# Kernel tuning notes

Hardware: AMD Instinct MI355X
Metric: run time of the kernel (lower is better)

Reference implementation:

```python
import jax, jax.numpy as jnp
import numpy as np

PATCH_SIZE = 24
ALPHA = 0.2  # LeakyReLU negative slope


def setup_inputs() -> dict:
    key = jax.random.key(0)
    k_x, k_adj, k_w, k_wc = jax.random.split(key, 4)
    B, T, N, Cin, Cout = 2, 96, 64, 16, 32
    x = jax.random.normal(k_x, (B, T, N, Cin), dtype=jnp.float32)
    adj = jax.random.uniform(k_adj, (N, N), dtype=jnp.float32)  # weighted adjacency in [0,1)
    # xavier_uniform with gain=1.414 on (Cin, Cout)
    limit = 1.414 * float(np.sqrt(6.0 / (Cin + Cout)))
    W = jax.random.uniform(k_w, (Cin, Cout), dtype=jnp.float32, minval=-limit, maxval=limit)
    W_c = jax.random.uniform(k_wc, (Cout,), dtype=jnp.float32, minval=-0.1, maxval=0.1)
    return {"x": x, "adj": adj, "W": W, "W_c": W_c}


def reference(x, adj, W, W_c):
    B, T, N, Cin = x.shape
    P = PATCH_SIZE
    NP = T // P
    Cout = W.shape[1]
    # torch.view semantics == row-major jnp.reshape (faithful, even though it mixes axes)
    x_patched = x.reshape(B, NP, N, P, Cin)
    h = x_patched @ W  # (B, NP, N, P, Cout)
    # vectorized over patches: per-patch outer product over nodes
    e = jnp.einsum('bsipc,bsjpc->bsijpc', h, h)  # (B, NP, N, N, P, Cout)
    e = jnp.where(e >= 0, e, ALPHA * e)  # LeakyReLU
    e = e * adj[None, None, :, :, None, None]
    e = jax.nn.softmax(e, axis=-1)  # softmax over channel dim (as in original)
    # torch.stack(list, dim=4) of (b,i,j,p,c) over patch index -> (B,N,N,P,NP,C)
    e = jnp.transpose(e, (0, 2, 3, 4, 1, 5))
    attention = e.reshape(B, N, N, T, Cout)  # (B, N, N, T, Cout)
    # h_patched.permute(0,2,1,3,4).reshape(B,N,T,C)
    h_flat = jnp.transpose(h, (0, 2, 1, 3, 4)).reshape(B, N, T, Cout)
    # einsum('bnqtc,bntc->bntc') == sum over q then elementwise multiply
    h_prime = attention.sum(axis=2) * h_flat
    return attention, jax.nn.elu(h_prime)
```

## Files before the change

### kernel.cpp

```cpp
#include <hip/hip_runtime.h>
#include <math.h>

#define Bq 2
#define Tq 96
#define Nq 64
#define CIN 16
#define COUT 32
#define PATCH 24
#define NPq 4
#define ATT_SIZE (Bq * Nq * Nq * Tq * COUT)
#define H_ROWS (Bq * NPq * Nq * PATCH)

typedef float f4 __attribute__((ext_vector_type(4)));

__global__ __launch_bounds__(256) void h_gemm_kernel(
    const float* __restrict__ x, const float* __restrict__ W,
    float* __restrict__ h) {
    __shared__ float Wl[CIN * COUT];
    __shared__ float xs[8 * CIN];
    int tid = threadIdx.x;
    Wl[tid]       = W[tid];
    Wl[tid + 256] = W[tid + 256];
    if (tid < 8 * CIN) xs[tid] = x[blockIdx.x * (8 * CIN) + tid];
    __syncthreads();
    int rl = tid >> 5;
    int c  = tid & 31;
    float acc = 0.f;
#pragma unroll
    for (int k = 0; k < CIN; ++k)
        acc += xs[rl * CIN + k] * Wl[k * COUT + c];
    h[blockIdx.x * 256 + tid] = acc;
}

__global__ __launch_bounds__(768) void att_fused_kernel(
    const float* __restrict__ h, const float* __restrict__ adj,
    float* __restrict__ att, float* __restrict__ hprime) {
    const int bi = blockIdx.x;
    const int s  = bi & 3;
    const int i  = (bi >> 2) & 63;
    const int b  = bi >> 8;
    const int tid  = threadIdx.x;
    const int c0   = (tid & 7) * 4;
    const int p    = (tid >> 3) % PATCH;
    const int jsub = tid / 192;
    const int j0   = jsub * 16;

    __shared__ float adjrow[Nq];
    __shared__ f4 red[768];
    if (tid < Nq) adjrow[tid] = adj[i * Nq + tid];
    __syncthreads();

    const float* hb = h + (size_t)((b * NPq + s) * Nq) * (PATCH * COUT);
    const f4 hi = *(const f4*)(hb + (i * PATCH + p) * COUT + c0);

    f4 acc = {0.f, 0.f, 0.f, 0.f};
    const int t = p * NPq + s;
    size_t outbase = ((size_t)((b * Nq + i) * Nq + j0) * Tq + t) * COUT + c0;
    const size_t jstride = (size_t)Tq * COUT;

#pragma unroll 4
    for (int jj = 0; jj < 16; ++jj) {
        const f4 hj = *(const f4*)(hb + ((j0 + jj) * PATCH + p) * COUT + c0);
        const float aj = adjrow[j0 + jj];

        f4 e = hi * hj;
        e.x = fmaxf(e.x, 0.2f * e.x) * aj;
        e.y = fmaxf(e.y, 0.2f * e.y) * aj;
        e.z = fmaxf(e.z, 0.2f * e.z) * aj;
        e.w = fmaxf(e.w, 0.2f * e.w) * aj;

        f4 ex;
        ex.x = __expf(e.x); ex.y = __expf(e.y);
        ex.z = __expf(e.z); ex.w = __expf(e.w);
        float sm = (ex.x + ex.y) + (ex.z + ex.w);
#pragma unroll
        for (int d = 1; d < 8; d <<= 1) sm += __shfl_xor(sm, d);
        const float inv = __builtin_amdgcn_rcpf(sm);
        f4 a = ex * inv;
        acc += a;
        *(f4*)(att + outbase + (size_t)jj * jstride) = a;
    }

    red[tid] = acc;
    __syncthreads();

    if (jsub == 0) {
        const f4 a0 = red[tid];
        const f4 a1 = red[tid + 192];
        const f4 a2 = red[tid + 384];
        const f4 a3 = red[tid + 576];
        f4 asum = (a0 + a1) + (a2 + a3);

        const int s2 = t / PATCH;
        const int p2 = t % PATCH;
        const f4 hv = *(const f4*)(h + (size_t)((b * NPq + s2) * Nq + i) * (PATCH * COUT)
                                     + p2 * COUT + c0);
        f4 v = asum * hv;
        v.x = v.x >= 0.f ? v.x : expm1f(v.x);
        v.y = v.y >= 0.f ? v.y : expm1f(v.y);
        v.z = v.z >= 0.f ? v.z : expm1f(v.z);
        v.w = v.w >= 0.f ? v.w : expm1f(v.w);
        *(f4*)(hprime + ((size_t)((b * Nq + i) * Tq + t)) * COUT + c0) = v;
    }
}

extern "C" void kernel_launch(void* const* d_in, const int* in_sizes, int n_in,
                              void* d_out, int out_size, void* d_ws, size_t ws_size,
                              hipStream_t stream) {
    (void)in_sizes; (void)n_in; (void)out_size; (void)ws_size;
    const float* x   = (const float*)d_in[0];
    const float* adj = (const float*)d_in[1];
    const float* W   = (const float*)d_in[2];

    float* h   = (float*)d_ws;
    float* att = (float*)d_out;
    float* hp  = (float*)d_out + ATT_SIZE;

    hipLaunchKernelGGL(h_gemm_kernel, dim3(H_ROWS / 8), dim3(256), 0, stream,
                       x, W, h);
    hipLaunchKernelGGL(att_fused_kernel, dim3(Bq * Nq * NPq), dim3(768), 0, stream,
                       h, adj, att, hp);
}
```

Measured before the change: 28.84 us.

## Remap attention kernel so each thread loops all j and writes contiguous t

Each block now covers one (b,i) and half of the time axis, and each thread handles one (t, 4-channel) slot and loops over all 64 neighbours j. The shared-memory reduction and its extra barrier go away. Consecutive threads now write consecutive t rows, so the attention stores are contiguous across the block. In exchange there are fewer blocks (256 instead of 512) and each thread runs a longer serial loop, which may reduce latency hiding.

```diff
diff --git a/kernel.cpp b/kernel.cpp
--- a/kernel.cpp
+++ b/kernel.cpp
@@ -10,6 +10,7 @@
 #define NPq 4
 #define ATT_SIZE (Bq * Nq * Nq * Tq * COUT)
 #define H_ROWS (Bq * NPq * Nq * PATCH)
+#define SLAB (Nq * PATCH * COUT)
 
 typedef float f4 __attribute__((ext_vector_type(4)));
 
@@ -32,36 +33,34 @@
     h[blockIdx.x * 256 + tid] = acc;
 }
 
-__global__ __launch_bounds__(768) void att_fused_kernel(
+__global__ __launch_bounds__(384) void att_fused_kernel(
     const float* __restrict__ h, const float* __restrict__ adj,
     float* __restrict__ att, float* __restrict__ hprime) {
     const int bi = blockIdx.x;
-    const int s  = bi & 3;
-    const int i  = (bi >> 2) & 63;
-    const int b  = bi >> 8;
-    const int tid  = threadIdx.x;
-    const int c0   = (tid & 7) * 4;
-    const int p    = (tid >> 3) % PATCH;
-    const int jsub = tid / 192;
-    const int j0   = jsub * 16;
+    const int th = bi & 1;
+    const int i  = (bi >> 1) & 63;
+    const int b  = bi >> 7;
+    const int tid = threadIdx.x;
+    const int c0  = (tid & 7) * 4;
+    const int t   = th * 48 + (tid >> 3);
+    const int s   = t & 3;
+    const int p   = t >> 2;
 
     __shared__ float adjrow[Nq];
-    __shared__ f4 red[768];
     if (tid < Nq) adjrow[tid] = adj[i * Nq + tid];
     __syncthreads();
 
-    const float* hb = h + (size_t)((b * NPq + s) * Nq) * (PATCH * COUT);
-    const f4 hi = *(const f4*)(hb + (i * PATCH + p) * COUT + c0);
+    const float* hslab = h + (size_t)(b * NPq + s) * SLAB;
+    const f4 hi = *(const f4*)(hslab + (i * PATCH + p) * COUT + c0);
 
     f4 acc = {0.f, 0.f, 0.f, 0.f};
-    const int t = p * NPq + s;
-    size_t outbase = ((size_t)((b * Nq + i) * Nq + j0) * Tq + t) * COUT + c0;
+    size_t outbase = ((size_t)((b * Nq + i) * Nq) * Tq + t) * COUT + c0;
     const size_t jstride = (size_t)Tq * COUT;
 
 #pragma unroll 4
-    for (int jj = 0; jj < 16; ++jj) {
-        const f4 hj = *(const f4*)(hb + ((j0 + jj) * PATCH + p) * COUT + c0);
-        const float aj = adjrow[j0 + jj];
+    for (int jj = 0; jj < Nq; ++jj) {
+        const f4 hj = *(const f4*)(hslab + (jj * PATCH + p) * COUT + c0);
+        const float aj = adjrow[jj];
 
         f4 e = hi * hj;
         e.x = fmaxf(e.x, 0.2f * e.x) * aj;
@@ -81,27 +80,16 @@
         *(f4*)(att + outbase + (size_t)jj * jstride) = a;
     }
 
-    red[tid] = acc;
-    __syncthreads();
-
-    if (jsub == 0) {
-        const f4 a0 = red[tid];
-        const f4 a1 = red[tid + 192];
-        const f4 a2 = red[tid + 384];
-        const f4 a3 = red[tid + 576];
-        f4 asum = (a0 + a1) + (a2 + a3);
-
-        const int s2 = t / PATCH;
-        const int p2 = t % PATCH;
-        const f4 hv = *(const f4*)(h + (size_t)((b * NPq + s2) * Nq + i) * (PATCH * COUT)
-                                     + p2 * COUT + c0);
-        f4 v = asum * hv;
-        v.x = v.x >= 0.f ? v.x : expm1f(v.x);
-        v.y = v.y >= 0.f ? v.y : expm1f(v.y);
-        v.z = v.z >= 0.f ? v.z : expm1f(v.z);
-        v.w = v.w >= 0.f ? v.w : expm1f(v.w);
-        *(f4*)(hprime + ((size_t)((b * Nq + i) * Tq + t)) * COUT + c0) = v;
-    }
+    const int s2 = t / PATCH;
+    const int p2 = t % PATCH;
+    const f4 hv = *(const f4*)(h + (size_t)((b * NPq + s2) * Nq + i) * (PATCH * COUT)
+                                 + p2 * COUT + c0);
+    f4 v = acc * hv;
+    v.x = v.x >= 0.f ? v.x : expm1f(v.x);
+    v.y = v.y >= 0.f ? v.y : expm1f(v.y);
+    v.z = v.z >= 0.f ? v.z : expm1f(v.z);
+    v.w = v.w >= 0.f ? v.w : expm1f(v.w);
+    *(f4*)(hprime + ((size_t)((b * Nq + i) * Tq + t)) * COUT + c0) = v;
 }
 
 extern "C" void kernel_launch(void* const* d_in, const int* in_sizes, int n_in,
@@ -118,6 +106,6 @@
 
     hipLaunchKernelGGL(h_gemm_kernel, dim3(H_ROWS / 8), dim3(256), 0, stream,
                        x, W, h);
-    hipLaunchKernelGGL(att_fused_kernel, dim3(Bq * Nq * NPq), dim3(768), 0, stream,
+    hipLaunchKernelGGL(att_fused_kernel, dim3(Bq * Nq * 2), dim3(384), 0, stream,
                        h, adj, att, hp);
 }
```

Result: slower. 29.56 us (+2.5%).

## Fuse h GEMM into attention kernel and process two rows i per block

Applied to the files above, without the earlier changes.

Removes the separate h GEMM launch and the workspace round-trip by recomputing h rows in registers from x and W inside the attention kernel. Each block now handles two source nodes i, so every recomputed hj vector is reused across both rows, and the grid is halved to 256 blocks of 768 threads. This trades the launch and global traffic for redundant GEMM arithmetic across blocks, heavier register use (16 hj plus 16 W vectors per thread), and lower block-level parallelism. The attention output write, about 50 MB, still dominates the work.

```diff
diff --git a/kernel.cpp b/kernel.cpp
--- a/kernel.cpp
+++ b/kernel.cpp
@@ -9,115 +9,142 @@
 #define PATCH 24
 #define NPq 4
 #define ATT_SIZE (Bq * Nq * Nq * Tq * COUT)
-#define H_ROWS (Bq * NPq * Nq * PATCH)
 
 typedef float f4 __attribute__((ext_vector_type(4)));
 
-__global__ __launch_bounds__(256) void h_gemm_kernel(
-    const float* __restrict__ x, const float* __restrict__ W,
-    float* __restrict__ h) {
-    __shared__ float Wl[CIN * COUT];
-    __shared__ float xs[8 * CIN];
-    int tid = threadIdx.x;
-    Wl[tid]       = W[tid];
-    Wl[tid + 256] = W[tid + 256];
-    if (tid < 8 * CIN) xs[tid] = x[blockIdx.x * (8 * CIN) + tid];
-    __syncthreads();
-    int rl = tid >> 5;
-    int c  = tid & 31;
-    float acc = 0.f;
+__global__ __launch_bounds__(768, 3) void gat_fused_kernel(
+    const float* __restrict__ x, const float* __restrict__ adj,
+    const float* __restrict__ W,
+    float* __restrict__ att, float* __restrict__ hprime) {
+  const int bi = blockIdx.x;
+  const int s  = bi & 3;
+  const int ig = (bi >> 2) & 31;
+  const int b  = bi >> 7;
+  const int i0 = ig * 2;
+  const int tid  = threadIdx.x;
+  const int c4   = tid & 7;
+  const int p    = (tid >> 3) % PATCH;
+  const int jsub = tid / 192;
+  const int j0   = jsub * 16;
+  const int t    = p * NPq + s;
+
+  __shared__ float adjr[2][Nq];
+  __shared__ f4 red[2][4][PATCH][8];
+
+  if (tid < 2 * Nq)
+    adjr[tid >> 6][tid & 63] = adj[(i0 + (tid >> 6)) * Nq + (tid & 63)];
+  __syncthreads();
+
+  const f4* x4 = (const f4*)x;
+  const f4* W4 = (const f4*)W;
+
+  f4 Wr[16];
 #pragma unroll
-    for (int k = 0; k < CIN; ++k)
-        acc += xs[rl * CIN + k] * Wl[k * COUT + c];
-    h[blockIdx.x * 256 + tid] = acc;
-}
+  for (int k = 0; k < 16; ++k) Wr[k] = W4[k * 8 + c4];
 
-__global__ __launch_bounds__(768) void att_fused_kernel(
-    const float* __restrict__ h, const float* __restrict__ adj,
-    float* __restrict__ att, float* __restrict__ hprime) {
-    const int bi = blockIdx.x;
-    const int s  = bi & 3;
-    const int i  = (bi >> 2) & 63;
-    const int b  = bi >> 8;
-    const int tid  = threadIdx.x;
-    const int c0   = (tid & 7) * 4;
-    const int p    = (tid >> 3) % PATCH;
-    const int jsub = tid / 192;
-    const int j0   = jsub * 16;
+  auto rowdot = [&](int row) -> f4 {
+    const f4 x0 = x4[row * 4 + 0], x1 = x4[row * 4 + 1];
+    const f4 x2 = x4[row * 4 + 2], x3 = x4[row * 4 + 3];
+    f4 a = x0.x * Wr[0];
+    a += x0.y * Wr[1];  a += x0.z * Wr[2];  a += x0.w * Wr[3];
+    a += x1.x * Wr[4];  a += x1.y * Wr[5];  a += x1.z * Wr[6];  a += x1.w * Wr[7];
+    a += x2.x * Wr[8];  a += x2.y * Wr[9];  a += x2.z * Wr[10]; a += x2.w * Wr[11];
+    a += x3.x * Wr[12]; a += x3.y * Wr[13]; a += x3.z * Wr[14]; a += x3.w * Wr[15];
+    return a;
+  };
 
-    __shared__ float adjrow[Nq];
-    __shared__ f4 red[768];
-    if (tid < Nq) adjrow[tid] = adj[i * Nq + tid];
-    __syncthreads();
+  const int rbase = (b * NPq + s) * Nq;
+  const int s2 = t / PATCH, p2 = t % PATCH;
 
-    const float* hb = h + (size_t)((b * NPq + s) * Nq) * (PATCH * COUT);
-    const f4 hi = *(const f4*)(hb + (i * PATCH + p) * COUT + c0);
+  const f4 hi0 = rowdot((rbase + i0) * PATCH + p);
+  const f4 hi1 = rowdot((rbase + i0 + 1) * PATCH + p);
+  const f4 hf0 = rowdot(((b * NPq + s2) * Nq + i0) * PATCH + p2);
+  const f4 hf1 = rowdot(((b * NPq + s2) * Nq + i0 + 1) * PATCH + p2);
 
-    f4 acc = {0.f, 0.f, 0.f, 0.f};
-    const int t = p * NPq + s;
-    size_t outbase = ((size_t)((b * Nq + i) * Nq + j0) * Tq + t) * COUT + c0;
-    const size_t jstride = (size_t)Tq * COUT;
+  f4 hj[16];
+#pragma unroll
+  for (int jj = 0; jj < 16; ++jj)
+    hj[jj] = rowdot((rbase + j0 + jj) * PATCH + p);
+
+  f4 acc0 = {0.f, 0.f, 0.f, 0.f};
+  f4 acc1 = {0.f, 0.f, 0.f, 0.f};
+  const int c0 = c4 * 4;
+  size_t ob0 = ((size_t)((b * Nq + i0) * Nq + j0) * Tq + t) * COUT + c0;
+  size_t ob1 = ob0 + (size_t)Nq * Tq * COUT;
+  const size_t jstride = (size_t)Tq * COUT;
 
 #pragma unroll 4
-    for (int jj = 0; jj < 16; ++jj) {
-        const f4 hj = *(const f4*)(hb + ((j0 + jj) * PATCH + p) * COUT + c0);
-        const float aj = adjrow[j0 + jj];
+  for (int jj = 0; jj < 16; ++jj) {
+    const f4 hjv = hj[jj];
+    const float a0 = adjr[0][j0 + jj];
+    const float a1 = adjr[1][j0 + jj];
+    {
+      f4 e = hi0 * hjv;
+      e.x = fmaxf(e.x, 0.2f * e.x) * a0;
+      e.y = fmaxf(e.y, 0.2f * e.y) * a0;
+      e.z = fmaxf(e.z, 0.2f * e.z) * a0;
+      e.w = fmaxf(e.w, 0.2f * e.w) * a0;
+      f4 ex;
+      ex.x = __expf(e.x); ex.y = __expf(e.y);
+      ex.z = __expf(e.z); ex.w = __expf(e.w);
+      float sm = (ex.x + ex.y) + (ex.z + ex.w);
+      sm += __shfl_xor(sm, 1); sm += __shfl_xor(sm, 2); sm += __shfl_xor(sm, 4);
+      f4 a = ex * __builtin_amdgcn_rcpf(sm);
+      acc0 += a;
+      *(f4*)(att + ob0 + (size_t)jj * jstride) = a;
+    }
+    {
+      f4 e = hi1 * hjv;
+      e.x = fmaxf(e.x, 0.2f * e.x) * a1;
+      e.y = fmaxf(e.y, 0.2f * e.y) * a1;
+      e.z = fmaxf(e.z, 0.2f * e.z) * a1;
+      e.w = fmaxf(e.w, 0.2f * e.w) * a1;
+      f4 ex;
+      ex.x = __expf(e.x); ex.y = __expf(e.y);
+      ex.z = __expf(e.z); ex.w = __expf(e.w);
+      float sm = (ex.x + ex.y) + (ex.z + ex.w);
+      sm += __shfl_xor(sm, 1); sm += __shfl_xor(sm, 2); sm += __shfl_xor(sm, 4);
+      f4 a = ex * __builtin_amdgcn_rcpf(sm);
+      acc1 += a;
+      *(f4*)(att + ob1 + (size_t)jj * jstride) = a;
+    }
+  }
 
-        f4 e = hi * hj;
-        e.x = fmaxf(e.x, 0.2f * e.x) * aj;
-        e.y = fmaxf(e.y, 0.2f * e.y) * aj;
-        e.z = fmaxf(e.z, 0.2f * e.z) * aj;
-        e.w = fmaxf(e.w, 0.2f * e.w) * aj;
+  red[0][jsub][p][c4] = acc0;
+  red[1][jsub][p][c4] = acc1;
+  __syncthreads();
 
-        f4 ex;
-        ex.x = __expf(e.x); ex.y = __expf(e.y);
-        ex.z = __expf(e.z); ex.w = __expf(e.w);
-        float sm = (ex.x + ex.y) + (ex.z + ex.w);
-#pragma unroll
-        for (int d = 1; d < 8; d <<= 1) sm += __shfl_xor(sm, d);
-        const float inv = __builtin_amdgcn_rcpf(sm);
-        f4 a = ex * inv;
-        acc += a;
-        *(f4*)(att + outbase + (size_t)jj * jstride) = a;
-    }
-
-    red[tid] = acc;
-    __syncthreads();
-
-    if (jsub == 0) {
-        const f4 a0 = red[tid];
-        const f4 a1 = red[tid + 192];
-        const f4 a2 = red[tid + 384];
-        const f4 a3 = red[tid + 576];
-        f4 asum = (a0 + a1) + (a2 + a3);
-
-        const int s2 = t / PATCH;
-        const int p2 = t % PATCH;
-        const f4 hv = *(const f4*)(h + (size_t)((b * NPq + s2) * Nq + i) * (PATCH * COUT)
-                                     + p2 * COUT + c0);
-        f4 v = asum * hv;
-        v.x = v.x >= 0.f ? v.x : expm1f(v.x);
-        v.y = v.y >= 0.f ? v.y : expm1f(v.y);
-        v.z = v.z >= 0.f ? v.z : expm1f(v.z);
-        v.w = v.w >= 0.f ? v.w : expm1f(v.w);
-        *(f4*)(hprime + ((size_t)((b * Nq + i) * Tq + t)) * COUT + c0) = v;
-    }
+  if (jsub == 0) {
+    f4 s0 = (red[0][0][p][c4] + red[0][1][p][c4]) +
+            (red[0][2][p][c4] + red[0][3][p][c4]);
+    f4 s1 = (red[1][0][p][c4] + red[1][1][p][c4]) +
+            (red[1][2][p][c4] + red[1][3][p][c4]);
+    f4 v0 = s0 * hf0;
+    f4 v1 = s1 * hf1;
+    v0.x = v0.x >= 0.f ? v0.x : expm1f(v0.x);
+    v0.y = v0.y >= 0.f ? v0.y : expm1f(v0.y);
+    v0.z = v0.z >= 0.f ? v0.z : expm1f(v0.z);
+    v0.w = v0.w >= 0.f ? v0.w : expm1f(v0.w);
+    v1.x = v1.x >= 0.f ? v1.x : expm1f(v1.x);
+    v1.y = v1.y >= 0.f ? v1.y : expm1f(v1.y);
+    v1.z = v1.z >= 0.f ? v1.z : expm1f(v1.z);
+    v1.w = v1.w >= 0.f ? v1.w : expm1f(v1.w);
+    *(f4*)(hprime + ((size_t)((b * Nq + i0) * Tq + t)) * COUT + c0) = v0;
+    *(f4*)(hprime + ((size_t)((b * Nq + i0 + 1) * Tq + t)) * COUT + c0) = v1;
+  }
 }
 
 extern "C" void kernel_launch(void* const* d_in, const int* in_sizes, int n_in,
                               void* d_out, int out_size, void* d_ws, size_t ws_size,
                               hipStream_t stream) {
-    (void)in_sizes; (void)n_in; (void)out_size; (void)ws_size;
-    const float* x   = (const float*)d_in[0];
-    const float* adj = (const float*)d_in[1];
-    const float* W   = (const float*)d_in[2];
+  (void)in_sizes; (void)n_in; (void)out_size; (void)d_ws; (void)ws_size;
+  const float* x   = (const float*)d_in[0];
+  const float* adj = (const float*)d_in[1];
+  const float* W   = (const float*)d_in[2];
 
-    float* h   = (float*)d_ws;
-    float* att = (float*)d_out;
-    float* hp  = (float*)d_out + ATT_SIZE;
+  float* att = (float*)d_out;
+  float* hp  = (float*)d_out + ATT_SIZE;
 
-    hipLaunchKernelGGL(h_gemm_kernel, dim3(H_ROWS / 8), dim3(256), 0, stream,
-                       x, W, h);
-    hipLaunchKernelGGL(att_fused_kernel, dim3(Bq * Nq * NPq), dim3(768), 0, stream,
-                       h, adj, att, hp);
+  hipLaunchKernelGGL(gat_fused_kernel, dim3(Bq * 32 * NPq), dim3(768), 0, stream,
+                     x, adj, W, att, hp);
 }
```

Result: slower. 44.12 us (+53.0%).

## Split attention into denominator pass and coalesced recompute-and-write pass

Applied to the files above, without the earlier changes.

The fused attention kernel becomes two kernels. The first computes the per-(j,t) softmax reciprocals and h_prime, storing the reciprocals in workspace. The second recomputes the exponentials with a block mapping that covers all time steps for a group of j, so each block writes contiguous attention rows. This trades an extra launch, recomputed exps and a small intermediate buffer for a more coalesced store pattern on the large attention output.

```diff
diff --git a/kernel.cpp b/kernel.cpp
--- a/kernel.cpp
+++ b/kernel.cpp
@@ -10,6 +10,8 @@
 #define NPq 4
 #define ATT_SIZE (Bq * Nq * Nq * Tq * COUT)
 #define H_ROWS (Bq * NPq * Nq * PATCH)
+#define SLAB (Nq * PATCH * COUT)
+#define INV_SIZE (Bq * Nq * Nq * Tq)
 
 typedef float f4 __attribute__((ext_vector_type(4)));
 
@@ -32,15 +34,16 @@
     h[blockIdx.x * 256 + tid] = acc;
 }
 
-__global__ __launch_bounds__(768) void att_fused_kernel(
+__global__ __launch_bounds__(768) void denom_kernel(
     const float* __restrict__ h, const float* __restrict__ adj,
-    float* __restrict__ att, float* __restrict__ hprime) {
+    float* __restrict__ inv, float* __restrict__ hprime) {
     const int bi = blockIdx.x;
     const int s  = bi & 3;
     const int i  = (bi >> 2) & 63;
     const int b  = bi >> 8;
     const int tid  = threadIdx.x;
-    const int c0   = (tid & 7) * 4;
+    const int c4   = tid & 7;
+    const int c0   = c4 * 4;
     const int p    = (tid >> 3) % PATCH;
     const int jsub = tid / 192;
     const int j0   = jsub * 16;
@@ -50,15 +53,14 @@
     if (tid < Nq) adjrow[tid] = adj[i * Nq + tid];
     __syncthreads();
 
-    const float* hb = h + (size_t)((b * NPq + s) * Nq) * (PATCH * COUT);
+    const float* hb = h + (size_t)(b * NPq + s) * SLAB;
     const f4 hi = *(const f4*)(hb + (i * PATCH + p) * COUT + c0);
 
     f4 acc = {0.f, 0.f, 0.f, 0.f};
     const int t = p * NPq + s;
-    size_t outbase = ((size_t)((b * Nq + i) * Nq + j0) * Tq + t) * COUT + c0;
-    const size_t jstride = (size_t)Tq * COUT;
+    const size_t invbase = ((size_t)((b * Nq + i) * Nq + j0)) * Tq + t;
 
-#pragma unroll 4
+#pragma unroll
     for (int jj = 0; jj < 16; ++jj) {
         const f4 hj = *(const f4*)(hb + ((j0 + jj) * PATCH + p) * COUT + c0);
         const float aj = adjrow[j0 + jj];
@@ -75,10 +77,9 @@
         float sm = (ex.x + ex.y) + (ex.z + ex.w);
 #pragma unroll
         for (int d = 1; d < 8; d <<= 1) sm += __shfl_xor(sm, d);
-        const float inv = __builtin_amdgcn_rcpf(sm);
-        f4 a = ex * inv;
-        acc += a;
-        *(f4*)(att + outbase + (size_t)jj * jstride) = a;
+        const float iv = __builtin_amdgcn_rcpf(sm);
+        acc += ex * iv;
+        if (c4 == 0) inv[invbase + (size_t)jj * Tq] = iv;
     }
 
     red[tid] = acc;
@@ -104,6 +105,47 @@
     }
 }
 
+__global__ __launch_bounds__(768) void attwrite_kernel(
+    const float* __restrict__ h, const float* __restrict__ adj,
+    const float* __restrict__ inv, float* __restrict__ att) {
+    const int g  = blockIdx.x;
+    const int jc = g & 7;
+    const int i  = (g >> 3) & 63;
+    const int b  = g >> 9;
+    const int j0 = jc * 8;
+    const int tid = threadIdx.x;
+    const int c0 = (tid & 7) * 4;
+    const int t  = tid >> 3;
+    const int s  = t & 3;
+    const int p  = t >> 2;
+
+    const float* hb = h + (size_t)(b * NPq + s) * SLAB;
+    const f4 hi = *(const f4*)(hb + (i * PATCH + p) * COUT + c0);
+
+    const size_t outbase = ((size_t)((b * Nq + i) * Nq + j0) * Tq + t) * COUT + c0;
+    const size_t jstride = (size_t)Tq * COUT;
+    const size_t invbase = ((size_t)((b * Nq + i) * Nq + j0)) * Tq + t;
+
+#pragma unroll
+    for (int jj = 0; jj < 8; ++jj) {
+        const float aj = adj[i * Nq + j0 + jj];
+        const f4 hj = *(const f4*)(hb + ((j0 + jj) * PATCH + p) * COUT + c0);
+
+        f4 e = hi * hj;
+        e.x = fmaxf(e.x, 0.2f * e.x) * aj;
+        e.y = fmaxf(e.y, 0.2f * e.y) * aj;
+        e.z = fmaxf(e.z, 0.2f * e.z) * aj;
+        e.w = fmaxf(e.w, 0.2f * e.w) * aj;
+
+        f4 ex;
+        ex.x = __expf(e.x); ex.y = __expf(e.y);
+        ex.z = __expf(e.z); ex.w = __expf(e.w);
+
+        const float iv = inv[invbase + (size_t)jj * Tq];
+        *(f4*)(att + outbase + (size_t)jj * jstride) = ex * iv;
+    }
+}
+
 extern "C" void kernel_launch(void* const* d_in, const int* in_sizes, int n_in,
                               void* d_out, int out_size, void* d_ws, size_t ws_size,
                               hipStream_t stream) {
@@ -113,11 +155,14 @@
     const float* W   = (const float*)d_in[2];
 
     float* h   = (float*)d_ws;
+    float* inv = (float*)d_ws + H_ROWS * COUT;
     float* att = (float*)d_out;
     float* hp  = (float*)d_out + ATT_SIZE;
 
     hipLaunchKernelGGL(h_gemm_kernel, dim3(H_ROWS / 8), dim3(256), 0, stream,
                        x, W, h);
-    hipLaunchKernelGGL(att_fused_kernel, dim3(Bq * Nq * NPq), dim3(768), 0, stream,
-                       h, adj, att, hp);
+    hipLaunchKernelGGL(denom_kernel, dim3(Bq * Nq * NPq), dim3(768), 0, stream,
+                       h, adj, inv, hp);
+    hipLaunchKernelGGL(attwrite_kernel, dim3(Bq * Nq * 8), dim3(768), 0, stream,
+                       h, adj, inv, att);
 }
```

Result: slower. 46.36 us (+60.8%).
